# Kernel tuning notes

Hardware: AMD Instinct MI355X
Metric: run time of the kernel (lower is better)

Reference implementation:

```python
import jax, jax.numpy as jnp
import numpy as np

C = 256   # channels
N = 512   # hidden (2*channels)
K = 15    # fixed-point iterations


def setup_inputs() -> dict:
    key = jax.random.key(0)
    ks = jax.random.split(key, 6)
    x = jax.random.normal(ks[0], (16, 4096, C), dtype=jnp.float32)
    # in_proj: Linear(C -> N), weight ~ N(0, 0.01), identity added to top-left CxC block
    W_in = jax.random.normal(ks[1], (N, C), dtype=jnp.float32) * 0.01
    W_in = W_in.at[:C, :C].add(jnp.eye(C, dtype=jnp.float32))
    b_in = jnp.zeros((N,), dtype=jnp.float32)
    # recurrent weight W ~ N(0, 0.01), bias b = 0
    W = jax.random.normal(ks[2], (N, N), dtype=jnp.float32) * 0.01
    b = jnp.zeros((N,), dtype=jnp.float32)
    # out_proj: Linear(N -> C), weight ~ N(0, 0.01), identity added to top-left CxC block
    W_out = jax.random.normal(ks[3], (C, N), dtype=jnp.float32) * 0.01
    W_out = W_out.at[:C, :C].add(jnp.eye(C, dtype=jnp.float32))
    b_out = jnp.zeros((C,), dtype=jnp.float32)
    return {"x": x, "W_in": W_in, "b_in": b_in, "W": W, "b": b,
            "W_out": W_out, "b_out": b_out}


def reference(x, W_in, b_in, W, b, W_out, b_out):
    B, L, Cc = x.shape
    x_flat = x.reshape(B * L, Cc)
    c = x_flat @ W_in.T + b_in            # (B*L, N) drive term
    Ws = 0.5 * (W + W.T)                  # symmetrize=True
    a0 = jnp.zeros_like(c)

    def step(a, _):
        a = jnp.tanh(a @ Ws.T + b + c)
        return a, None

    a, _ = jax.lax.scan(step, a0, None, length=K)
    y_flat = a @ W_out.T + b_out          # (B*L, C)
    return y_flat.reshape(B, L, Cc)
```

## Files before the change

### kernel.cpp

```cpp
#include <hip/hip_runtime.h>


using bf16x8 = __attribute__((ext_vector_type(8))) __bf16;
using f32x16 = __attribute__((ext_vector_type(16))) float;
using i32x4  = __attribute__((ext_vector_type(4))) int;
using i32x16 = __attribute__((ext_vector_type(16))) int;

__device__ __forceinline__ unsigned int pack2bf(float a, float b) {
  unsigned int ua = __builtin_bit_cast(unsigned int, a);
  unsigned int ub = __builtin_bit_cast(unsigned int, b);
  return ((ua + 0x8000u) >> 16) | ((ub + 0x8000u) & 0xffff0000u);
}

__device__ __forceinline__ unsigned short f2bf(float v) {
  unsigned int u = __builtin_bit_cast(unsigned int, v);
  return (unsigned short)((u + 0x7fffu + ((u >> 16) & 1u)) >> 16);
}

__device__ __forceinline__ float fast_tanh(float x) {
  float e = __builtin_amdgcn_exp2f(x * 2.885390082f);
  float r = __builtin_amdgcn_rcpf(e + 1.0f);
  return __builtin_fmaf(-2.0f, r, 1.0f);
}

__device__ __forceinline__ f32x16 mfma_bf(uint4 a, uint4 b, f32x16 c) {
  return __builtin_amdgcn_mfma_f32_32x32x16_bf16(
      __builtin_bit_cast(bf16x8, a), __builtin_bit_cast(bf16x8, b), c, 0, 0, 0);
}

__device__ __forceinline__ i32x16 mfma_i8(uint4 a, uint4 b, i32x16 c) {
  return __builtin_amdgcn_mfma_i32_32x32x32_i8(
      __builtin_bit_cast(i32x4, a), __builtin_bit_cast(i32x4, b), c, 0, 0, 0);
}

__device__ __forceinline__ unsigned int q8pack(float t0, float t1, float t2, float t3) {
  int q0 = (int)__builtin_rintf(t0 * 127.f);
  int q1 = (int)__builtin_rintf(t1 * 127.f);
  int q2 = (int)__builtin_rintf(t2 * 127.f);
  int q3 = (int)__builtin_rintf(t3 * 127.f);
  return (q0 & 255) | ((q1 & 255) << 8) | ((q2 & 255) << 16) | ((unsigned)q3 << 24);
}

__global__ void prep(const float* __restrict__ W,
                     const float* __restrict__ Win,
                     const float* __restrict__ Wout,
                     signed char* __restrict__ WsI8,
                     signed char* __restrict__ WoutRI8,
                     unsigned short* __restrict__ WinBf) {
  int t = blockIdx.x * 256 + threadIdx.x;
  if (t < 262144) {
    int j = t & 15, L = (t >> 4) & 63, mtG = (t >> 10) & 15, s = (t >> 14) & 15;
    int m = mtG * 32 + (L & 31);
    int k = s * 32 + (L >> 5) * 16 + j;
    float v = __builtin_rintf(0.5f * (W[m * 512 + k] + W[k * 512 + m]) * 2048.f);
    v = fminf(127.f, fmaxf(-127.f, v));
    WsI8[t] = (signed char)(int)v;
  } else if (t < 393216) {
    WinBf[t - 262144] = f2bf(Win[t - 262144]);
  } else {
    int u = t - 393216;
    int j = u & 15, L = (u >> 4) & 63, wv = (u >> 10) & 7, s = (u >> 13) & 15;
    int m = wv * 32 + (L & 31);
    int k = s * 32 + (L >> 5) * 16 + j;
    float r = Wout[m * 512 + k] - ((m == k) ? 1.f : 0.f);
    r = fminf(127.f, fmaxf(-127.f, __builtin_rintf(r * 2048.f)));
    WoutRI8[u] = (signed char)(int)r;
  }
}

__global__ __launch_bounds__(512, 4) void attractor_kernel(
    const float* __restrict__ x,
    const unsigned short* __restrict__ WinBf,
    const float* __restrict__ binf,
    const float* __restrict__ brecf,
    const signed char* __restrict__ WoutRI8,
    const float* __restrict__ boutf,
    const signed char* __restrict__ WsI8,
    float* __restrict__ y)
{
  __shared__ uint4 smem4[4160];
  char* aC = (char*)smem4;

  const int tid  = threadIdx.x;
  const int lane = tid & 63;
  const int w    = tid >> 6;
  const int il   = lane & 31;
  const int g    = lane >> 5;
  const int sw   = w * 2;
  const int blk  = blockIdx.x;

  const float4* __restrict__ xf4  = (const float4*)x;
  const uint4* __restrict__ Win4  = (const uint4*)WinBf;
  uint4* __restrict__ y4 = (uint4*)y;

  unsigned int c_pk[2][2][8];

  auto storeA = [&](int base, int mt, int nt, int p, unsigned int pk) {
    const int u = w * 4 + mt * 2 + (p >> 1);
    *(unsigned int*)(aC + base + (nt * 32 + il) * 512 +
                     ((u ^ il) << 4) + 8 * (p & 1) + 4 * g) = pk;
  };

  {
    f32x16 accf[2][2];
    #pragma unroll
    for (int mt = 0; mt < 2; ++mt)
      #pragma unroll
      for (int nt = 0; nt < 2; ++nt)
        #pragma unroll
        for (int r = 0; r < 16; ++r) accf[mt][nt][r] = 0.0f;

    #pragma unroll 2
    for (int s = 0; s < 16; ++s) {
      uint4 A[2], B[2];
      #pragma unroll
      for (int mt = 0; mt < 2; ++mt) {
        int m = w * 64 + mt * 32 + il;
        A[mt] = Win4[m * 32 + 2 * s + g];
      }
      #pragma unroll
      for (int nt = 0; nt < 2; ++nt) {
        int i = blk * 64 + nt * 32 + il;
        float4 f0 = xf4[i * 64 + 4 * s + 2 * g + 0];
        float4 f1 = xf4[i * 64 + 4 * s + 2 * g + 1];
        B[nt].x = pack2bf(f0.x, f0.y);
        B[nt].y = pack2bf(f0.z, f0.w);
        B[nt].z = pack2bf(f1.x, f1.y);
        B[nt].w = pack2bf(f1.z, f1.w);
      }
      #pragma unroll
      for (int mt = 0; mt < 2; ++mt)
        #pragma unroll
        for (int nt = 0; nt < 2; ++nt)
          accf[mt][nt] = mfma_bf(A[mt], B[nt], accf[mt][nt]);
    }

    #pragma unroll
    for (int mt = 0; mt < 2; ++mt) {
      #pragma unroll
      for (int p = 0; p < 4; ++p) {
        const int n0 = w * 64 + mt * 32 + 8 * p + 4 * g;
        float b0 = binf[n0 + 0] + brecf[n0 + 0];
        float b1 = binf[n0 + 1] + brecf[n0 + 1];
        float b2 = binf[n0 + 2] + brecf[n0 + 2];
        float b3 = binf[n0 + 3] + brecf[n0 + 3];
        #pragma unroll
        for (int nt = 0; nt < 2; ++nt) {
          float v0 = accf[mt][nt][4 * p + 0] + b0;
          float v1 = accf[mt][nt][4 * p + 1] + b1;
          float v2 = accf[mt][nt][4 * p + 2] + b2;
          float v3 = accf[mt][nt][4 * p + 3] + b3;
          c_pk[mt][nt][2 * p + 0] = pack2bf(2.885390082f * v0, 2.885390082f * v1);
          c_pk[mt][nt][2 * p + 1] = pack2bf(2.885390082f * v2, 2.885390082f * v3);
          storeA(0, mt, nt, p, q8pack(fast_tanh(v0), fast_tanh(v1),
                                      fast_tanh(v2), fast_tanh(v3)));
        }
      }
    }
  }

  const uint4* Ws4 = (const uint4*)WsI8;
  const uint4* pA = Ws4 + (2 * w) * 64 + lane;
  uint4 Ab[2][2];
  Ab[0][0] = pA[sw * 1024];
  Ab[0][1] = pA[sw * 1024 + 64];

  __syncthreads();

  const float SE = 2.885390082f / 260096.f;
  const float QM = 12583039.0f;
  const int rdBase = il * 512;

  #pragma unroll 1
  for (int it = 0; it < 14; ++it) {
    i32x16 acc[2][2];
    #pragma unroll
    for (int mt = 0; mt < 2; ++mt)
      #pragma unroll
      for (int nt = 0; nt < 2; ++nt)
        #pragma unroll
        for (int r = 0; r < 16; ++r) acc[mt][nt][r] = 0;

    const int rb = (it & 1) << 15;

    #pragma unroll 2
    for (int s = 0; s < 16; ++s) {
      const int se = (s + sw) & 15;
      const int sn = (s + 1 + sw) & 15;
      Ab[(s + 1) & 1][0] = pA[sn * 1024];
      Ab[(s + 1) & 1][1] = pA[sn * 1024 + 64];
      const int bu = rb + rdBase + (((2 * se + g) ^ il) << 4);
      uint4 B0 = *(const uint4*)(aC + bu);
      uint4 B1 = *(const uint4*)(aC + bu + 16384);
      acc[0][0] = mfma_i8(Ab[s & 1][0], B0, acc[0][0]);
      acc[0][1] = mfma_i8(Ab[s & 1][0], B1, acc[0][1]);
      acc[1][0] = mfma_i8(Ab[s & 1][1], B0, acc[1][0]);
      acc[1][1] = mfma_i8(Ab[s & 1][1], B1, acc[1][1]);
    }

    const int wb = rb ^ 32768;
    #pragma unroll
    for (int mt = 0; mt < 2; ++mt)
      #pragma unroll
      for (int nt = 0; nt < 2; ++nt)
        #pragma unroll
        for (int p = 0; p < 4; ++p) {
          unsigned u01 = c_pk[mt][nt][2 * p + 0];
          unsigned u23 = c_pk[mt][nt][2 * p + 1];
          float c0 = __builtin_bit_cast(float, u01 << 16);
          float c1 = __builtin_bit_cast(float, u01 & 0xffff0000u);
          float c2 = __builtin_bit_cast(float, u23 << 16);
          float c3 = __builtin_bit_cast(float, u23 & 0xffff0000u);
          float e0 = __builtin_amdgcn_exp2f(__builtin_fmaf((float)acc[mt][nt][4 * p + 0], SE, c0));
          float e1 = __builtin_amdgcn_exp2f(__builtin_fmaf((float)acc[mt][nt][4 * p + 1], SE, c1));
          float e2 = __builtin_amdgcn_exp2f(__builtin_fmaf((float)acc[mt][nt][4 * p + 2], SE, c2));
          float e3 = __builtin_amdgcn_exp2f(__builtin_fmaf((float)acc[mt][nt][4 * p + 3], SE, c3));
          float r0 = __builtin_amdgcn_rcpf(e0 + 1.0f);
          float r1 = __builtin_amdgcn_rcpf(e1 + 1.0f);
          float r2 = __builtin_amdgcn_rcpf(e2 + 1.0f);
          float r3 = __builtin_amdgcn_rcpf(e3 + 1.0f);
          unsigned f0 = __builtin_bit_cast(unsigned, __builtin_fmaf(-254.f, r0, QM));
          unsigned f1 = __builtin_bit_cast(unsigned, __builtin_fmaf(-254.f, r1, QM));
          unsigned f2 = __builtin_bit_cast(unsigned, __builtin_fmaf(-254.f, r2, QM));
          unsigned f3 = __builtin_bit_cast(unsigned, __builtin_fmaf(-254.f, r3, QM));
          unsigned pk = (f0 & 0xffu) | ((f1 & 0xffu) << 8) |
                        ((f2 & 0xffu) << 16) | (f3 << 24);
          storeA(wb, mt, nt, p, pk);
        }
    __syncthreads();
  }

  const float S = 1.f / 260096.f;
  const uint4* Wr4 = (const uint4*)WoutRI8;
  const uint4* pR = Wr4 + w * 64 + lane;
  i32x16 o[2];
  #pragma unroll
  for (int nt = 0; nt < 2; ++nt)
    #pragma unroll
    for (int r = 0; r < 16; ++r) o[nt][r] = 0;

  #pragma unroll 2
  for (int s = 0; s < 16; ++s) {
    const int se = (s + sw) & 15;
    uint4 A = pR[se * 512];
    const int bu = rdBase + (((2 * se + g) ^ il) << 4);
    uint4 B0 = *(const uint4*)(aC + bu);
    uint4 B1 = *(const uint4*)(aC + bu + 16384);
    o[0] = mfma_i8(A, B0, o[0]);
    o[1] = mfma_i8(A, B1, o[1]);
  }

  #pragma unroll
  for (int nt = 0; nt < 2; ++nt) {
    const int rowb = (nt * 32 + il) * 512;
    uint4 Q0 = *(const uint4*)(aC + rowb + (((2 * w + 0) ^ il) << 4));
    uint4 Q1 = *(const uint4*)(aC + rowb + (((2 * w + 1) ^ il) << 4));
    #pragma unroll
    for (int p = 0; p < 4; ++p) {
      const int c0i = w * 32 + 8 * p + 4 * g;
      float4 bo = *(const float4*)(boutf + c0i);
      unsigned lo, hi;
      if      (p == 0) { lo = Q0.x; hi = Q0.y; }
      else if (p == 1) { lo = Q0.z; hi = Q0.w; }
      else if (p == 2) { lo = Q1.x; hi = Q1.y; }
      else             { lo = Q1.z; hi = Q1.w; }
      const unsigned wrd = g ? hi : lo;
      #pragma unroll
      for (int q = 0; q < 4; ++q) {
        int aq = (int)(signed char)(wrd >> (8 * q));
        float bq = (q == 0) ? bo.x : (q == 1) ? bo.y : (q == 2) ? bo.z : bo.w;
        float yv = __builtin_fmaf((float)o[nt][4 * p + q], S,
                   __builtin_fmaf((float)aq, 1.f / 127.f, bq));
        o[nt][4 * p + q] = __builtin_bit_cast(int, yv);
      }
    }
  }
  __syncthreads();

  uint4* yst4 = smem4;
  #pragma unroll
  for (int p = 0; p < 4; ++p) {
    const int c0 = w * 32 + 8 * p + 4 * g;
    #pragma unroll
    for (int nt = 0; nt < 2; ++nt) {
      const int irow = nt * 32 + il;
      uint4 r;
      r.x = (unsigned)o[nt][4 * p + 0];
      r.y = (unsigned)o[nt][4 * p + 1];
      r.z = (unsigned)o[nt][4 * p + 2];
      r.w = (unsigned)o[nt][4 * p + 3];
      yst4[irow * 65 + (c0 >> 2)] = r;
    }
  }
  __syncthreads();

  #pragma unroll
  for (int p = 0; p < 8; ++p) {
    int idx = p * 512 + tid;
    int row = idx >> 6;
    int col = idx & 63;
    y4[(blk * 64 + row) * 64 + col] = yst4[row * 65 + col];
  }
}

extern "C" void kernel_launch(void* const* d_in, const int* in_sizes, int n_in,
                              void* d_out, int out_size, void* d_ws, size_t ws_size,
                              hipStream_t stream) {
  const float* x    = (const float*)d_in[0];
  const float* Win  = (const float*)d_in[1];
  const float* bin  = (const float*)d_in[2];
  const float* W    = (const float*)d_in[3];
  const float* brec = (const float*)d_in[4];
  const float* Wout = (const float*)d_in[5];
  const float* bout = (const float*)d_in[6];

  signed char* WsI8       = (signed char*)d_ws;
  signed char* WoutRI8    = WsI8 + 262144;
  unsigned short* WinBf   = (unsigned short*)(WsI8 + 393216);

  prep<<<2048, 256, 0, stream>>>(W, Win, Wout, WsI8, WoutRI8, WinBf);
  attractor_kernel<<<1024, 512, 0, stream>>>(x, WinBf, bin, brec, WoutRI8, bout,
                                             WsI8, (float*)d_out);
}
```

Before: 597.4 us.

## Software-pipeline recurrence across two token half-sets to overlap tanh epilogue with MFMA

Splits the 64-token block into two independent 32-token sets, each with its own single activation buffer. Each phase runs the int8 MFMA matmul for one set while interleaving the exp/rcp tanh epilogue and quantized store for the other set. The aim is to hide the transcendental epilogue latency behind matrix work instead of running it serially after each iteration. The cost is a more complex schedule, a fully unrolled inner loop and more live registers, which could lower occupancy or cause spills.

Result: slower. 1.852 ms (+209.9%).

```diff
diff --git a/kernel.cpp b/kernel.cpp
--- a/kernel.cpp
+++ b/kernel.cpp
@@ -95,10 +95,9 @@
 
   unsigned int c_pk[2][2][8];
 
-  auto storeA = [&](int base, int mt, int nt, int p, unsigned int pk) {
+  auto storeA = [&](int sb, int mt, int p, unsigned int pk) {
     const int u = w * 4 + mt * 2 + (p >> 1);
-    *(unsigned int*)(aC + base + (nt * 32 + il) * 512 +
-                     ((u ^ il) << 4) + 8 * (p & 1) + 4 * g) = pk;
+    *(unsigned int*)(aC + sb + il * 512 + ((u ^ il) << 4) + 8 * (p & 1) + 4 * g) = pk;
   };
 
   {
@@ -106,9 +105,9 @@
     #pragma unroll
     for (int mt = 0; mt < 2; ++mt)
       #pragma unroll
-      for (int nt = 0; nt < 2; ++nt)
+      for (int ss = 0; ss < 2; ++ss)
         #pragma unroll
-        for (int r = 0; r < 16; ++r) accf[mt][nt][r] = 0.0f;
+        for (int r = 0; r < 16; ++r) accf[mt][ss][r] = 0.0f;
 
     #pragma unroll 2
     for (int s = 0; s < 16; ++s) {
@@ -119,20 +118,20 @@
         A[mt] = Win4[m * 32 + 2 * s + g];
       }
       #pragma unroll
-      for (int nt = 0; nt < 2; ++nt) {
-        int i = blk * 64 + nt * 32 + il;
+      for (int ss = 0; ss < 2; ++ss) {
+        int i = blk * 64 + ss * 32 + il;
         float4 f0 = xf4[i * 64 + 4 * s + 2 * g + 0];
         float4 f1 = xf4[i * 64 + 4 * s + 2 * g + 1];
-        B[nt].x = pack2bf(f0.x, f0.y);
-        B[nt].y = pack2bf(f0.z, f0.w);
-        B[nt].z = pack2bf(f1.x, f1.y);
-        B[nt].w = pack2bf(f1.z, f1.w);
+        B[ss].x = pack2bf(f0.x, f0.y);
+        B[ss].y = pack2bf(f0.z, f0.w);
+        B[ss].z = pack2bf(f1.x, f1.y);
+        B[ss].w = pack2bf(f1.z, f1.w);
       }
       #pragma unroll
       for (int mt = 0; mt < 2; ++mt)
         #pragma unroll
-        for (int nt = 0; nt < 2; ++nt)
-          accf[mt][nt] = mfma_bf(A[mt], B[nt], accf[mt][nt]);
+        for (int ss = 0; ss < 2; ++ss)
+          accf[mt][ss] = mfma_bf(A[mt], B[ss], accf[mt][ss]);
     }
 
     #pragma unroll
@@ -145,15 +144,15 @@
         float b2 = binf[n0 + 2] + brecf[n0 + 2];
         float b3 = binf[n0 + 3] + brecf[n0 + 3];
         #pragma unroll
-        for (int nt = 0; nt < 2; ++nt) {
-          float v0 = accf[mt][nt][4 * p + 0] + b0;
-          float v1 = accf[mt][nt][4 * p + 1] + b1;
-          float v2 = accf[mt][nt][4 * p + 2] + b2;
-          float v3 = accf[mt][nt][4 * p + 3] + b3;
-          c_pk[mt][nt][2 * p + 0] = pack2bf(2.885390082f * v0, 2.885390082f * v1);
-          c_pk[mt][nt][2 * p + 1] = pack2bf(2.885390082f * v2, 2.885390082f * v3);
-          storeA(0, mt, nt, p, q8pack(fast_tanh(v0), fast_tanh(v1),
-                                      fast_tanh(v2), fast_tanh(v3)));
+        for (int ss = 0; ss < 2; ++ss) {
+          float v0 = accf[mt][ss][4 * p + 0] + b0;
+          float v1 = accf[mt][ss][4 * p + 1] + b1;
+          float v2 = accf[mt][ss][4 * p + 2] + b2;
+          float v3 = accf[mt][ss][4 * p + 3] + b3;
+          c_pk[mt][ss][2 * p + 0] = pack2bf(2.885390082f * v0, 2.885390082f * v1);
+          c_pk[mt][ss][2 * p + 1] = pack2bf(2.885390082f * v2, 2.885390082f * v3);
+          storeA(ss * 16384, mt, p, q8pack(fast_tanh(v0), fast_tanh(v1),
+                                           fast_tanh(v2), fast_tanh(v3)));
         }
       }
     }
@@ -171,73 +170,112 @@
   const float QM = 12583039.0f;
   const int rdBase = il * 512;
 
-  #pragma unroll 1
-  for (int it = 0; it < 14; ++it) {
-    i32x16 acc[2][2];
-    #pragma unroll
-    for (int mt = 0; mt < 2; ++mt)
-      #pragma unroll
-      for (int nt = 0; nt < 2; ++nt)
-        #pragma unroll
-        for (int r = 0; r < 16; ++r) acc[mt][nt][r] = 0;
-
-    const int rb = (it & 1) << 15;
-
+  i32x16 zA[2], zB[2];
+
+  auto phaseM = [&](i32x16 (&accM)[2], int sbR) {
+    #pragma unroll
+    for (int r = 0; r < 16; ++r) { accM[0][r] = 0; accM[1][r] = 0; }
     #pragma unroll 2
     for (int s = 0; s < 16; ++s) {
       const int se = (s + sw) & 15;
       const int sn = (s + 1 + sw) & 15;
-      Ab[(s + 1) & 1][0] = pA[sn * 1024];
-      Ab[(s + 1) & 1][1] = pA[sn * 1024 + 64];
-      const int bu = rb + rdBase + (((2 * se + g) ^ il) << 4);
-      uint4 B0 = *(const uint4*)(aC + bu);
-      uint4 B1 = *(const uint4*)(aC + bu + 16384);
-      acc[0][0] = mfma_i8(Ab[s & 1][0], B0, acc[0][0]);
-      acc[0][1] = mfma_i8(Ab[s & 1][0], B1, acc[0][1]);
-      acc[1][0] = mfma_i8(Ab[s & 1][1], B0, acc[1][0]);
-      acc[1][1] = mfma_i8(Ab[s & 1][1], B1, acc[1][1]);
-    }
-
-    const int wb = rb ^ 32768;
+      uint4 An0 = pA[sn * 1024];
+      uint4 An1 = pA[sn * 1024 + 64];
+      uint4 B = *(const uint4*)(aC + sbR + rdBase + (((2 * se + g) ^ il) << 4));
+      accM[0] = mfma_i8(Ab[s & 1][0], B, accM[0]);
+      accM[1] = mfma_i8(Ab[s & 1][1], B, accM[1]);
+      Ab[(s + 1) & 1][0] = An0;
+      Ab[(s + 1) & 1][1] = An1;
+    }
+  };
+
+  auto phaseFull = [&](i32x16 (&accM)[2], int sbR,
+                       i32x16 (&zE)[2], int setE, int sbW) {
+    #pragma unroll
+    for (int r = 0; r < 16; ++r) { accM[0][r] = 0; accM[1][r] = 0; }
+    unsigned carry = 0;
+    #pragma unroll
+    for (int s = 0; s < 16; ++s) {
+      const int se = (s + sw) & 15;
+      const int sn = (s + 1 + sw) & 15;
+      uint4 An0 = pA[sn * 1024];
+      uint4 An1 = pA[sn * 1024 + 64];
+      uint4 B = *(const uint4*)(aC + sbR + rdBase + (((2 * se + g) ^ il) << 4));
+      accM[0] = mfma_i8(Ab[s & 1][0], B, accM[0]);
+      accM[1] = mfma_i8(Ab[s & 1][1], B, accM[1]);
+      Ab[(s + 1) & 1][0] = An0;
+      Ab[(s + 1) & 1][1] = An1;
+      const int mt_e = s >> 3, j = s & 7, p = j >> 1, h = j & 1;
+      unsigned cw = c_pk[mt_e][setE][j];
+      float c0 = __builtin_bit_cast(float, cw << 16);
+      float c1 = __builtin_bit_cast(float, cw & 0xffff0000u);
+      float e0 = __builtin_amdgcn_exp2f(
+          __builtin_fmaf((float)zE[mt_e][4 * p + 2 * h + 0], SE, c0));
+      float e1 = __builtin_amdgcn_exp2f(
+          __builtin_fmaf((float)zE[mt_e][4 * p + 2 * h + 1], SE, c1));
+      float r0 = __builtin_amdgcn_rcpf(e0 + 1.0f);
+      float r1 = __builtin_amdgcn_rcpf(e1 + 1.0f);
+      unsigned f0 = __builtin_bit_cast(unsigned, __builtin_fmaf(-254.f, r0, QM));
+      unsigned f1 = __builtin_bit_cast(unsigned, __builtin_fmaf(-254.f, r1, QM));
+      unsigned two = (f0 & 0xffu) | ((f1 & 0xffu) << 8);
+      if (h == 0) {
+        carry = two;
+      } else {
+        storeA(sbW, mt_e, p, carry | (two << 16));
+      }
+    }
+  };
+
+  auto epiOnly = [&](i32x16 (&zE)[2], int setE, int sbW) {
     #pragma unroll
     for (int mt = 0; mt < 2; ++mt)
       #pragma unroll
-      for (int nt = 0; nt < 2; ++nt)
-        #pragma unroll
-        for (int p = 0; p < 4; ++p) {
-          unsigned u01 = c_pk[mt][nt][2 * p + 0];
-          unsigned u23 = c_pk[mt][nt][2 * p + 1];
-          float c0 = __builtin_bit_cast(float, u01 << 16);
-          float c1 = __builtin_bit_cast(float, u01 & 0xffff0000u);
-          float c2 = __builtin_bit_cast(float, u23 << 16);
-          float c3 = __builtin_bit_cast(float, u23 & 0xffff0000u);
-          float e0 = __builtin_amdgcn_exp2f(__builtin_fmaf((float)acc[mt][nt][4 * p + 0], SE, c0));
-          float e1 = __builtin_amdgcn_exp2f(__builtin_fmaf((float)acc[mt][nt][4 * p + 1], SE, c1));
-          float e2 = __builtin_amdgcn_exp2f(__builtin_fmaf((float)acc[mt][nt][4 * p + 2], SE, c2));
-          float e3 = __builtin_amdgcn_exp2f(__builtin_fmaf((float)acc[mt][nt][4 * p + 3], SE, c3));
-          float r0 = __builtin_amdgcn_rcpf(e0 + 1.0f);
-          float r1 = __builtin_amdgcn_rcpf(e1 + 1.0f);
-          float r2 = __builtin_amdgcn_rcpf(e2 + 1.0f);
-          float r3 = __builtin_amdgcn_rcpf(e3 + 1.0f);
-          unsigned f0 = __builtin_bit_cast(unsigned, __builtin_fmaf(-254.f, r0, QM));
-          unsigned f1 = __builtin_bit_cast(unsigned, __builtin_fmaf(-254.f, r1, QM));
-          unsigned f2 = __builtin_bit_cast(unsigned, __builtin_fmaf(-254.f, r2, QM));
-          unsigned f3 = __builtin_bit_cast(unsigned, __builtin_fmaf(-254.f, r3, QM));
-          unsigned pk = (f0 & 0xffu) | ((f1 & 0xffu) << 8) |
-                        ((f2 & 0xffu) << 16) | (f3 << 24);
-          storeA(wb, mt, nt, p, pk);
-        }
+      for (int p = 0; p < 4; ++p) {
+        unsigned u01 = c_pk[mt][setE][2 * p + 0];
+        unsigned u23 = c_pk[mt][setE][2 * p + 1];
+        float c0 = __builtin_bit_cast(float, u01 << 16);
+        float c1 = __builtin_bit_cast(float, u01 & 0xffff0000u);
+        float c2 = __builtin_bit_cast(float, u23 << 16);
+        float c3 = __builtin_bit_cast(float, u23 & 0xffff0000u);
+        float e0 = __builtin_amdgcn_exp2f(__builtin_fmaf((float)zE[mt][4 * p + 0], SE, c0));
+        float e1 = __builtin_amdgcn_exp2f(__builtin_fmaf((float)zE[mt][4 * p + 1], SE, c1));
+        float e2 = __builtin_amdgcn_exp2f(__builtin_fmaf((float)zE[mt][4 * p + 2], SE, c2));
+        float e3 = __builtin_amdgcn_exp2f(__builtin_fmaf((float)zE[mt][4 * p + 3], SE, c3));
+        float r0 = __builtin_amdgcn_rcpf(e0 + 1.0f);
+        float r1 = __builtin_amdgcn_rcpf(e1 + 1.0f);
+        float r2 = __builtin_amdgcn_rcpf(e2 + 1.0f);
+        float r3 = __builtin_amdgcn_rcpf(e3 + 1.0f);
+        unsigned f0 = __builtin_bit_cast(unsigned, __builtin_fmaf(-254.f, r0, QM));
+        unsigned f1 = __builtin_bit_cast(unsigned, __builtin_fmaf(-254.f, r1, QM));
+        unsigned f2 = __builtin_bit_cast(unsigned, __builtin_fmaf(-254.f, r2, QM));
+        unsigned f3 = __builtin_bit_cast(unsigned, __builtin_fmaf(-254.f, r3, QM));
+        storeA(sbW, mt, p, (f0 & 0xffu) | ((f1 & 0xffu) << 8) |
+                           ((f2 & 0xffu) << 16) | (f3 << 24));
+      }
+  };
+
+  phaseM(zA, 0);
+  __syncthreads();
+  #pragma unroll 1
+  for (int k = 1; k <= 14; ++k) {
+    phaseFull(zB, 16384, zA, 0, 0);
     __syncthreads();
-  }
+    if (k < 14) {
+      phaseFull(zA, 0, zB, 1, 16384);
+      __syncthreads();
+    }
+  }
+  epiOnly(zB, 1, 16384);
+  __syncthreads();
 
   const float S = 1.f / 260096.f;
   const uint4* Wr4 = (const uint4*)WoutRI8;
   const uint4* pR = Wr4 + w * 64 + lane;
   i32x16 o[2];
   #pragma unroll
-  for (int nt = 0; nt < 2; ++nt)
-    #pragma unroll
-    for (int r = 0; r < 16; ++r) o[nt][r] = 0;
+  for (int ss = 0; ss < 2; ++ss)
+    #pragma unroll
+    for (int r = 0; r < 16; ++r) o[ss][r] = 0;
 
   #pragma unroll 2
   for (int s = 0; s < 16; ++s) {
@@ -251,8 +289,8 @@
   }
 
   #pragma unroll
-  for (int nt = 0; nt < 2; ++nt) {
-    const int rowb = (nt * 32 + il) * 512;
+  for (int ss = 0; ss < 2; ++ss) {
+    const int rowb = ss * 16384 + il * 512;
     uint4 Q0 = *(const uint4*)(aC + rowb + (((2 * w + 0) ^ il) << 4));
     uint4 Q1 = *(const uint4*)(aC + rowb + (((2 * w + 1) ^ il) << 4));
     #pragma unroll
@@ -269,9 +307,9 @@
       for (int q = 0; q < 4; ++q) {
         int aq = (int)(signed char)(wrd >> (8 * q));
         float bq = (q == 0) ? bo.x : (q == 1) ? bo.y : (q == 2) ? bo.z : bo.w;
-        float yv = __builtin_fmaf((float)o[nt][4 * p + q], S,
+        float yv = __builtin_fmaf((float)o[ss][4 * p + q], S,
                    __builtin_fmaf((float)aq, 1.f / 127.f, bq));
-        o[nt][4 * p + q] = __builtin_bit_cast(int, yv);
+        o[ss][4 * p + q] = __builtin_bit_cast(int, yv);
       }
     }
   }
@@ -282,13 +320,13 @@
   for (int p = 0; p < 4; ++p) {
     const int c0 = w * 32 + 8 * p + 4 * g;
     #pragma unroll
-    for (int nt = 0; nt < 2; ++nt) {
-      const int irow = nt * 32 + il;
+    for (int ss = 0; ss < 2; ++ss) {
+      const int irow = ss * 32 + il;
       uint4 r;
-      r.x = (unsigned)o[nt][4 * p + 0];
-      r.y = (unsigned)o[nt][4 * p + 1];
-      r.z = (unsigned)o[nt][4 * p + 2];
-      r.w = (unsigned)o[nt][4 * p + 3];
+      r.x = (unsigned)o[ss][4 * p + 0];
+      r.y = (unsigned)o[ss][4 * p + 1];
+      r.z = (unsigned)o[ss][4 * p + 2];
+      r.w = (unsigned)o[ss][4 * p + 3];
       yst4[irow * 65 + (c0 >> 2)] = r;
     }
   }
```
